# Optimization experiments

Measured on AMD Instinct MI355X. Metric: run time of the kernel, lower is better.

## Reference

```python
import jax, jax.numpy as jnp
import numpy as np

P_CLASSES = 1024   # num_classes_per_batch
K_SAMP = 4         # num_samples_per_class
MARGIN = 1.0
EPS = 1e-6
EMBED_DIM = 128


def setup_inputs() -> dict:
    key = jax.random.key(0)
    x = jax.random.normal(key, (P_CLASSES * K_SAMP, EMBED_DIM), dtype=jnp.float32)
    return {"x": x}


def reference(x):
    p, k = P_CLASSES, K_SAMP
    n = p * k
    # pairwise distances D[i,j] = sqrt(relu(|xi|^2 - 2 xi.xj + |xj|^2) + eps)
    norms = jnp.sum(x * x, axis=1)
    D = norms[:, None] - 2.0 * (x @ x.T) + norms[None, :]
    D = jnp.sqrt(jax.nn.relu(D) + EPS)  # [n, n]

    # all positive pairs (i<j) within each class, vectorized over classes
    ii, jj = np.triu_indices(k, 1)                      # [m], m = k*(k-1)/2
    c = np.arange(p)
    ri = (c[:, None] * k + ii[None, :]).reshape(-1)     # [P] = [p*m]
    rj = (c[:, None] * k + jj[None, :]).reshape(-1)
    pair_cls = np.repeat(c, len(ii))                    # class of each pair
    col_cls = np.arange(n) // k                         # class of each column
    neg_mask = jnp.asarray(pair_cls[:, None] != col_cls[None, :])  # [P, n]

    # masked logsumexp over negatives from both anchor rows (concat of the
    # two sliced rows in the original code)
    rows = jnp.concatenate([D[ri], D[rj]], axis=1)                 # [P, 2n]
    mask2 = jnp.concatenate([neg_mask, neg_mask], axis=1)
    vals = jnp.where(mask2, MARGIN - rows, -jnp.inf)
    lse = jax.scipy.special.logsumexp(vals, axis=1)                # [P]

    J = lse + D[ri, rj]
    return jnp.mean(jnp.square(jax.nn.relu(J))) / 2.0
```

## Files before the change

### kernel.cpp

```cpp
#include <hip/hip_runtime.h>

#define NROWS 4096
#define DIM 128
#define PCLS 1024
#define NPAIR 6144
#define MARGIN 1.0f
#define EPS 1e-6f

typedef __attribute__((ext_vector_type(8))) short bf16x8;
typedef __attribute__((ext_vector_type(4))) float f32x4;

union FragU { uint4 u; bf16x8 v; };

__device__ __forceinline__ unsigned short f2bf(float f) {
    unsigned int b = __float_as_uint(f);
    b = (b + 0x7FFFu + ((b >> 16) & 1u)) >> 16;
    return (unsigned short)b;
}

__global__ void prep_kernel(const float* __restrict__ x,
                            unsigned short* __restrict__ xbf,
                            float* __restrict__ norms) {
    int row = blockIdx.x * 4 + (threadIdx.x >> 6);
    int l = threadIdx.x & 63;
    float2 v = *reinterpret_cast<const float2*>(x + row * DIM + 2 * l);
    unsigned int packed = (unsigned int)f2bf(v.x) | ((unsigned int)f2bf(v.y) << 16);
    *reinterpret_cast<unsigned int*>(xbf + row * DIM + 2 * l) = packed;
    float s = v.x * v.x + v.y * v.y;
    #pragma unroll
    for (int m = 1; m < 64; m <<= 1) s += __shfl_xor(s, m, 64);
    if (l == 0) norms[row] = s;
}

__launch_bounds__(512, 4)
__global__ void main_kernel(const unsigned short* __restrict__ xbf,
                            const float* __restrict__ norms,
                            float* __restrict__ partial,
                            float* __restrict__ posD) {
    __shared__ __align__(16) unsigned short lds[256 * DIM];
    const int t = threadIdx.x;
    const int w = t >> 6;
    const int l = t & 63;
    const int rb = blockIdx.x >> 4;
    const int cs = blockIdx.x & 15;
    const int rbase = rb * 128 + w * 16;
    const int cbase = cs * 256;
    const int lg = l >> 4;
    const int lr = l & 15;

    FragU afr[4];
    const char* abase = (const char*)xbf + (size_t)(rbase + lr) * 256 + lg * 16;
    #pragma unroll
    for (int s = 0; s < 4; ++s)
        afr[s].u = *reinterpret_cast<const uint4*>(abase + s * 64);

    float njv[16];
    #pragma unroll
    for (int tile = 0; tile < 16; ++tile)
        njv[tile] = norms[cbase + tile * 16 + lr];

    float ni[4];
    #pragma unroll
    for (int rr = 0; rr < 4; ++rr) ni[rr] = norms[rbase + lg * 4 + rr];

    #pragma unroll
    for (int it = 0; it < 8; ++it) {
        int lin = it * 8192 + t * 16;
        int col = lin >> 8;
        int inner = lin & 255;
        uint4 v = *reinterpret_cast<const uint4*>(
            (const char*)xbf + (size_t)(cbase + col) * 256 + inner);
        *reinterpret_cast<uint4*>(
            (char*)lds + col * 256 + (inner ^ ((col & 7) << 4))) = v;
    }

    __syncthreads();

    float accS[4] = {0.f, 0.f, 0.f, 0.f};

    #pragma unroll
    for (int tile = 0; tile < 16; ++tile) {
        const int lcol = tile * 16 + lr;
        const float nj = njv[tile];
        const char* bbase = (const char*)lds + lcol * 256;
        const int xr = (lcol & 7) << 4;
        f32x4 acc = {0.f, 0.f, 0.f, 0.f};
        #pragma unroll
        for (int s = 0; s < 4; ++s) {
            FragU bu;
            int inner = s * 64 + lg * 16;
            bu.u = *reinterpret_cast<const uint4*>(bbase + (inner ^ xr));
            acc = __builtin_amdgcn_mfma_f32_16x16x32_bf16(afr[s].v, bu.v, acc, 0, 0, 0);
        }
        const bool diag = (cbase + tile * 16) == rbase;
        if (!diag) {
            #pragma unroll
            for (int rr = 0; rr < 4; ++rr) {
                float nn = ni[rr] + nj;
                float d2 = fmaf(-2.0f, acc[rr], nn);
                float d = __builtin_amdgcn_sqrtf(fmaxf(d2, 0.f) + EPS);
                accS[rr] += __expf(MARGIN - d);
            }
        } else {
            #pragma unroll
            for (int rr = 0; rr < 4; ++rr) {
                int a = lg * 4 + rr;
                int b = lr;
                float nn = ni[rr] + nj;
                float d2 = fmaf(-2.0f, acc[rr], nn);
                float d = __builtin_amdgcn_sqrtf(fmaxf(d2, 0.f) + EPS);
                bool same = (a >> 2) == (b >> 2);
                accS[rr] += same ? 0.f : __expf(MARGIN - d);
                if (same && a < b) {
                    int i = a & 3, j = b & 3;
                    int idx = i * (7 - i) / 2 + (j - i - 1);
                    int cls = (rbase + a) >> 2;
                    posD[cls * 6 + idx] = d;
                }
            }
        }
    }
    #pragma unroll
    for (int rr = 0; rr < 4; ++rr) {
        #pragma unroll
        for (int m = 1; m < 16; m <<= 1) accS[rr] += __shfl_xor(accS[rr], m, 64);
    }
    if (lr == 0) {
        #pragma unroll
        for (int rr = 0; rr < 4; ++rr)
            partial[cs * NROWS + rbase + lg * 4 + rr] = accS[rr];
    }
}

__global__ void tail_kernel(const float* __restrict__ partial,
                            const float* __restrict__ posD,
                            float* __restrict__ out) {
    const int c = threadIdx.x;
    float S[4] = {0.f, 0.f, 0.f, 0.f};
    #pragma unroll
    for (int sp = 0; sp < 16; ++sp) {
        float4 v = *reinterpret_cast<const float4*>(partial + sp * NROWS + 4 * c);
        S[0] += v.x; S[1] += v.y; S[2] += v.z; S[3] += v.w;
    }
    const int II[6] = {0, 0, 0, 1, 1, 2};
    const int JJ[6] = {1, 2, 3, 2, 3, 3};
    float acc = 0.f;
    #pragma unroll
    for (int p = 0; p < 6; ++p) {
        float d = posD[c * 6 + p];
        float J = __logf(S[II[p]] + S[JJ[p]]) + d;
        float r = fmaxf(J, 0.f);
        acc += r * r;
    }
    #pragma unroll
    for (int m = 1; m < 64; m <<= 1) acc += __shfl_xor(acc, m, 64);
    __shared__ float red[16];
    if ((c & 63) == 0) red[c >> 6] = acc;
    __syncthreads();
    if (c < 64) {
        float v = (c < 16) ? red[c] : 0.f;
        #pragma unroll
        for (int m = 1; m < 16; m <<= 1) v += __shfl_xor(v, m, 64);
        if (c == 0) out[0] = v * (1.0f / (2.0f * (float)NPAIR));
    }
}

extern "C" void kernel_launch(void* const* d_in, const int* in_sizes, int n_in,
                              void* d_out, int out_size, void* d_ws, size_t ws_size,
                              hipStream_t stream) {
    const float* x = (const float*)d_in[0];
    char* ws = (char*)d_ws;
    unsigned short* xbf = (unsigned short*)ws;
    float* norms = (float*)(ws + 1048576);
    float* partial = (float*)(ws + 1048576 + 16384);
    float* posD = (float*)(ws + 1048576 + 16384 + 262144);
    float* out = (float*)d_out;

    hipLaunchKernelGGL(prep_kernel, dim3(NROWS / 4), dim3(256), 0, stream, x, xbf, norms);
    hipLaunchKernelGGL(main_kernel, dim3(512), dim3(512), 0, stream, xbf, norms, partial, posD);
    hipLaunchKernelGGL(tail_kernel, dim3(1), dim3(1024), 0, stream, partial, posD, out);
}
```

Baseline: 24.60 us.

## Retile main kernel to 256x128 blocks with two row subtiles per wave

Changes the block tile from 128 rows x 256 columns to 256 rows x 128 columns, so each wave holds two 16-row A fragments and reuses every LDS B fragment for two MFMAs. The LDS footprint halves and the column split doubles to 32 slices, so the tail kernel now sums 32 partials and the posD workspace offset moves. It also folds EPS into the norms and computes exp as exp2 with a single FMA. The cost is more registers per thread under the 512x4 launch bounds and twice the partial-sum traffic.

```diff
diff --git a/kernel.cpp b/kernel.cpp
--- a/kernel.cpp
+++ b/kernel.cpp
@@ -6,6 +6,7 @@
 #define NPAIR 6144
 #define MARGIN 1.0f
 #define EPS 1e-6f
+#define LOG2E 1.4426950408889634f
 
 typedef __attribute__((ext_vector_type(8))) short bf16x8;
 typedef __attribute__((ext_vector_type(4))) float f32x4;
@@ -37,34 +38,41 @@
                             const float* __restrict__ norms,
                             float* __restrict__ partial,
                             float* __restrict__ posD) {
-    __shared__ __align__(16) unsigned short lds[256 * DIM];
+    __shared__ __align__(16) unsigned short lds[128 * DIM];
     const int t = threadIdx.x;
     const int w = t >> 6;
     const int l = t & 63;
-    const int rb = blockIdx.x >> 4;
-    const int cs = blockIdx.x & 15;
-    const int rbase = rb * 128 + w * 16;
-    const int cbase = cs * 256;
+    const int rb = blockIdx.x >> 5;
+    const int cs = blockIdx.x & 31;
+    const int rbase = rb * 256 + w * 32;
+    const int cbase = cs * 128;
     const int lg = l >> 4;
     const int lr = l & 15;
 
-    FragU afr[4];
-    const char* abase = (const char*)xbf + (size_t)(rbase + lr) * 256 + lg * 16;
+    FragU afr[8];
     #pragma unroll
-    for (int s = 0; s < 4; ++s)
-        afr[s].u = *reinterpret_cast<const uint4*>(abase + s * 64);
+    for (int sub = 0; sub < 2; ++sub) {
+        const char* abase = (const char*)xbf +
+            (size_t)(rbase + sub * 16 + lr) * 256 + lg * 16;
+        #pragma unroll
+        for (int s = 0; s < 4; ++s)
+            afr[sub * 4 + s].u = *reinterpret_cast<const uint4*>(abase + s * 64);
+    }
 
-    float njv[16];
+    float njv[8];
     #pragma unroll
-    for (int tile = 0; tile < 16; ++tile)
+    for (int tile = 0; tile < 8; ++tile)
         njv[tile] = norms[cbase + tile * 16 + lr];
 
-    float ni[4];
+    float ni[8];
     #pragma unroll
-    for (int rr = 0; rr < 4; ++rr) ni[rr] = norms[rbase + lg * 4 + rr];
+    for (int sub = 0; sub < 2; ++sub)
+        #pragma unroll
+        for (int rr = 0; rr < 4; ++rr)
+            ni[sub * 4 + rr] = norms[rbase + sub * 16 + lg * 4 + rr] + EPS;
 
     #pragma unroll
-    for (int it = 0; it < 8; ++it) {
+    for (int it = 0; it < 4; ++it) {
         int lin = it * 8192 + t * 16;
         int col = lin >> 8;
         int inner = lin & 255;
@@ -76,59 +84,68 @@
 
     __syncthreads();
 
-    float accS[4] = {0.f, 0.f, 0.f, 0.f};
+    float accS[8] = {0.f, 0.f, 0.f, 0.f, 0.f, 0.f, 0.f, 0.f};
 
     #pragma unroll
-    for (int tile = 0; tile < 16; ++tile) {
+    for (int tile = 0; tile < 8; ++tile) {
         const int lcol = tile * 16 + lr;
         const float nj = njv[tile];
         const char* bbase = (const char*)lds + lcol * 256;
         const int xr = (lcol & 7) << 4;
-        f32x4 acc = {0.f, 0.f, 0.f, 0.f};
+        f32x4 acc0 = {0.f, 0.f, 0.f, 0.f};
+        f32x4 acc1 = {0.f, 0.f, 0.f, 0.f};
         #pragma unroll
         for (int s = 0; s < 4; ++s) {
             FragU bu;
             int inner = s * 64 + lg * 16;
             bu.u = *reinterpret_cast<const uint4*>(bbase + (inner ^ xr));
-            acc = __builtin_amdgcn_mfma_f32_16x16x32_bf16(afr[s].v, bu.v, acc, 0, 0, 0);
+            acc0 = __builtin_amdgcn_mfma_f32_16x16x32_bf16(afr[s].v, bu.v, acc0, 0, 0, 0);
+            acc1 = __builtin_amdgcn_mfma_f32_16x16x32_bf16(afr[4 + s].v, bu.v, acc1, 0, 0, 0);
         }
-        const bool diag = (cbase + tile * 16) == rbase;
-        if (!diag) {
-            #pragma unroll
-            for (int rr = 0; rr < 4; ++rr) {
-                float nn = ni[rr] + nj;
-                float d2 = fmaf(-2.0f, acc[rr], nn);
-                float d = __builtin_amdgcn_sqrtf(fmaxf(d2, 0.f) + EPS);
-                accS[rr] += __expf(MARGIN - d);
-            }
-        } else {
-            #pragma unroll
-            for (int rr = 0; rr < 4; ++rr) {
-                int a = lg * 4 + rr;
-                int b = lr;
-                float nn = ni[rr] + nj;
-                float d2 = fmaf(-2.0f, acc[rr], nn);
-                float d = __builtin_amdgcn_sqrtf(fmaxf(d2, 0.f) + EPS);
-                bool same = (a >> 2) == (b >> 2);
-                accS[rr] += same ? 0.f : __expf(MARGIN - d);
-                if (same && a < b) {
-                    int i = a & 3, j = b & 3;
-                    int idx = i * (7 - i) / 2 + (j - i - 1);
-                    int cls = (rbase + a) >> 2;
-                    posD[cls * 6 + idx] = d;
+        #pragma unroll
+        for (int sub = 0; sub < 2; ++sub) {
+            const f32x4& acc = sub ? acc1 : acc0;
+            const bool diag = (cbase + tile * 16) == (rbase + sub * 16);
+            if (!diag) {
+                #pragma unroll
+                for (int rr = 0; rr < 4; ++rr) {
+                    float nn = ni[sub * 4 + rr] + nj;
+                    float d2 = fmaf(-2.0f, acc[rr], nn);
+                    float d = __builtin_amdgcn_sqrtf(fmaxf(d2, EPS));
+                    accS[sub * 4 + rr] += __builtin_amdgcn_exp2f(fmaf(d, -LOG2E, LOG2E));
+                }
+            } else {
+                #pragma unroll
+                for (int rr = 0; rr < 4; ++rr) {
+                    int a = lg * 4 + rr;
+                    int b = lr;
+                    float nn = ni[sub * 4 + rr] + nj;
+                    float d2 = fmaf(-2.0f, acc[rr], nn);
+                    float d = __builtin_amdgcn_sqrtf(fmaxf(d2, EPS));
+                    float e = __builtin_amdgcn_exp2f(fmaf(d, -LOG2E, LOG2E));
+                    bool same = (a >> 2) == (b >> 2);
+                    accS[sub * 4 + rr] += same ? 0.f : e;
+                    if (same && a < b) {
+                        int i = a & 3, j = b & 3;
+                        int idx = i * (7 - i) / 2 + (j - i - 1);
+                        int cls = (rbase + sub * 16 + a) >> 2;
+                        posD[cls * 6 + idx] = d;
+                    }
                 }
             }
         }
     }
     #pragma unroll
-    for (int rr = 0; rr < 4; ++rr) {
+    for (int i = 0; i < 8; ++i) {
         #pragma unroll
-        for (int m = 1; m < 16; m <<= 1) accS[rr] += __shfl_xor(accS[rr], m, 64);
+        for (int m = 1; m < 16; m <<= 1) accS[i] += __shfl_xor(accS[i], m, 64);
     }
     if (lr == 0) {
         #pragma unroll
-        for (int rr = 0; rr < 4; ++rr)
-            partial[cs * NROWS + rbase + lg * 4 + rr] = accS[rr];
+        for (int sub = 0; sub < 2; ++sub)
+            #pragma unroll
+            for (int rr = 0; rr < 4; ++rr)
+                partial[cs * NROWS + rbase + sub * 16 + lg * 4 + rr] = accS[sub * 4 + rr];
     }
 }
 
@@ -138,7 +155,7 @@
     const int c = threadIdx.x;
     float S[4] = {0.f, 0.f, 0.f, 0.f};
     #pragma unroll
-    for (int sp = 0; sp < 16; ++sp) {
+    for (int sp = 0; sp < 32; ++sp) {
         float4 v = *reinterpret_cast<const float4*>(partial + sp * NROWS + 4 * c);
         S[0] += v.x; S[1] += v.y; S[2] += v.z; S[3] += v.w;
     }
@@ -173,7 +190,7 @@
     unsigned short* xbf = (unsigned short*)ws;
     float* norms = (float*)(ws + 1048576);
     float* partial = (float*)(ws + 1048576 + 16384);
-    float* posD = (float*)(ws + 1048576 + 16384 + 262144);
+    float* posD = (float*)(ws + 1048576 + 16384 + 524288);
     float* out = (float*)d_out;
 
     hipLaunchKernelGGL(prep_kernel, dim3(NROWS / 4), dim3(256), 0, stream, x, xbf, norms);
```

Measured after the change: 26.88 us. 1.09x slower.

## Exploit distance matrix symmetry by computing only upper-triangular 128x128 tiles

Applied to the files above, without the earlier changes.

The main kernel now computes only the upper-triangular 128x128 blocks of the symmetric distance matrix, 528 blocks in place of 512 blocks of 128x256. Each off-diagonal block adds exp sums both across rows and down columns, with the column sums reduced across waves through shared memory. This roughly halves the MFMA and transcendental work. The exp is rewritten as exp2 with folded constants, and the partial sums are stored as bf16 to shrink the tail kernel's reads. The cost is an extra column reduction with a __syncthreads, more partial slices for the tail to sum, and bf16 rounding error in the partial sums.

```diff
diff --git a/kernel.cpp b/kernel.cpp
--- a/kernel.cpp
+++ b/kernel.cpp
@@ -6,6 +6,8 @@
 #define NPAIR 6144
 #define MARGIN 1.0f
 #define EPS 1e-6f
+#define LOG2E 1.4426950408889634f
+#define NSPLIT 32
 
 typedef __attribute__((ext_vector_type(8))) short bf16x8;
 typedef __attribute__((ext_vector_type(4))) float f32x4;
@@ -16,6 +18,9 @@
     unsigned int b = __float_as_uint(f);
     b = (b + 0x7FFFu + ((b >> 16) & 1u)) >> 16;
     return (unsigned short)b;
+}
+__device__ __forceinline__ float bf2f(unsigned short u) {
+    return __uint_as_float((unsigned int)u << 16);
 }
 
 __global__ void prep_kernel(const float* __restrict__ x,
@@ -35,36 +40,44 @@
 __launch_bounds__(512, 4)
 __global__ void main_kernel(const unsigned short* __restrict__ xbf,
                             const float* __restrict__ norms,
-                            float* __restrict__ partial,
+                            unsigned short* __restrict__ partial,
                             float* __restrict__ posD) {
-    __shared__ __align__(16) unsigned short lds[256 * DIM];
+    __shared__ __align__(16) unsigned short lds[128 * DIM];
+    __shared__ float colW[8 * 128];
     const int t = threadIdx.x;
     const int w = t >> 6;
     const int l = t & 63;
-    const int rb = blockIdx.x >> 4;
-    const int cs = blockIdx.x & 15;
-    const int rbase = rb * 128 + w * 16;
-    const int cbase = cs * 256;
     const int lg = l >> 4;
     const int lr = l & 15;
 
+    int u = blockIdx.x;
+    int rb = (int)((65.0f - sqrtf(4225.0f - 8.0f * (float)u)) * 0.5f);
+    while (rb > 0 && rb * (65 - rb) / 2 > u) --rb;
+    while ((rb + 1) * (64 - rb) / 2 <= u) ++rb;
+    const int cb = rb + (u - rb * (65 - rb) / 2);
+    const bool offd = (cb != rb);
+
+    const int rbase = rb * 128 + w * 16;
+    const int cbase = cb * 128;
+
     FragU afr[4];
     const char* abase = (const char*)xbf + (size_t)(rbase + lr) * 256 + lg * 16;
     #pragma unroll
     for (int s = 0; s < 4; ++s)
         afr[s].u = *reinterpret_cast<const uint4*>(abase + s * 64);
 
-    float njv[16];
-    #pragma unroll
-    for (int tile = 0; tile < 16; ++tile)
+    float njv[8];
+    #pragma unroll
+    for (int tile = 0; tile < 8; ++tile)
         njv[tile] = norms[cbase + tile * 16 + lr];
 
     float ni[4];
     #pragma unroll
-    for (int rr = 0; rr < 4; ++rr) ni[rr] = norms[rbase + lg * 4 + rr];
-
-    #pragma unroll
-    for (int it = 0; it < 8; ++it) {
+    for (int rr = 0; rr < 4; ++rr)
+        ni[rr] = norms[rbase + lg * 4 + rr] + EPS;
+
+    #pragma unroll
+    for (int it = 0; it < 4; ++it) {
         int lin = it * 8192 + t * 16;
         int col = lin >> 8;
         int inner = lin & 255;
@@ -77,9 +90,10 @@
     __syncthreads();
 
     float accS[4] = {0.f, 0.f, 0.f, 0.f};
-
-    #pragma unroll
-    for (int tile = 0; tile < 16; ++tile) {
+    float colA[8];
+
+    #pragma unroll
+    for (int tile = 0; tile < 8; ++tile) {
         const int lcol = tile * 16 + lr;
         const float nj = njv[tile];
         const char* bbase = (const char*)lds + lcol * 256;
@@ -92,14 +106,25 @@
             bu.u = *reinterpret_cast<const uint4*>(bbase + (inner ^ xr));
             acc = __builtin_amdgcn_mfma_f32_16x16x32_bf16(afr[s].v, bu.v, acc, 0, 0, 0);
         }
-        const bool diag = (cbase + tile * 16) == rbase;
-        if (!diag) {
+        if (offd) {
+            float es = 0.f;
             #pragma unroll
             for (int rr = 0; rr < 4; ++rr) {
                 float nn = ni[rr] + nj;
                 float d2 = fmaf(-2.0f, acc[rr], nn);
-                float d = __builtin_amdgcn_sqrtf(fmaxf(d2, 0.f) + EPS);
-                accS[rr] += __expf(MARGIN - d);
+                float d = __builtin_amdgcn_sqrtf(fmaxf(d2, EPS));
+                float e = __builtin_amdgcn_exp2f(fmaf(d, -LOG2E, LOG2E));
+                accS[rr] += e;
+                es += e;
+            }
+            colA[tile] = es;
+        } else if (tile != w) {
+            #pragma unroll
+            for (int rr = 0; rr < 4; ++rr) {
+                float nn = ni[rr] + nj;
+                float d2 = fmaf(-2.0f, acc[rr], nn);
+                float d = __builtin_amdgcn_sqrtf(fmaxf(d2, EPS));
+                accS[rr] += __builtin_amdgcn_exp2f(fmaf(d, -LOG2E, LOG2E));
             }
         } else {
             #pragma unroll
@@ -108,9 +133,10 @@
                 int b = lr;
                 float nn = ni[rr] + nj;
                 float d2 = fmaf(-2.0f, acc[rr], nn);
-                float d = __builtin_amdgcn_sqrtf(fmaxf(d2, 0.f) + EPS);
+                float d = __builtin_amdgcn_sqrtf(fmaxf(d2, EPS));
+                float e = __builtin_amdgcn_exp2f(fmaf(d, -LOG2E, LOG2E));
                 bool same = (a >> 2) == (b >> 2);
-                accS[rr] += same ? 0.f : __expf(MARGIN - d);
+                accS[rr] += same ? 0.f : e;
                 if (same && a < b) {
                     int i = a & 3, j = b & 3;
                     int idx = i * (7 - i) / 2 + (j - i - 1);
@@ -120,6 +146,7 @@
             }
         }
     }
+
     #pragma unroll
     for (int rr = 0; rr < 4; ++rr) {
         #pragma unroll
@@ -128,19 +155,39 @@
     if (lr == 0) {
         #pragma unroll
         for (int rr = 0; rr < 4; ++rr)
-            partial[cs * NROWS + rbase + lg * 4 + rr] = accS[rr];
-    }
-}
-
-__global__ void tail_kernel(const float* __restrict__ partial,
+            partial[cb * NROWS + rbase + lg * 4 + rr] = f2bf(accS[rr]);
+    }
+
+    if (offd) {
+        #pragma unroll
+        for (int tile = 0; tile < 8; ++tile) {
+            colA[tile] += __shfl_xor(colA[tile], 16, 64);
+            colA[tile] += __shfl_xor(colA[tile], 32, 64);
+        }
+        if (l < 16) {
+            #pragma unroll
+            for (int tile = 0; tile < 8; ++tile)
+                colW[w * 128 + tile * 16 + l] = colA[tile];
+        }
+        __syncthreads();
+        if (t < 128) {
+            float s = 0.f;
+            #pragma unroll
+            for (int ww = 0; ww < 8; ++ww) s += colW[ww * 128 + t];
+            partial[rb * NROWS + cbase + t] = f2bf(s);
+        }
+    }
+}
+
+__global__ void tail_kernel(const unsigned short* __restrict__ partial,
                             const float* __restrict__ posD,
                             float* __restrict__ out) {
     const int c = threadIdx.x;
     float S[4] = {0.f, 0.f, 0.f, 0.f};
     #pragma unroll
-    for (int sp = 0; sp < 16; ++sp) {
-        float4 v = *reinterpret_cast<const float4*>(partial + sp * NROWS + 4 * c);
-        S[0] += v.x; S[1] += v.y; S[2] += v.z; S[3] += v.w;
+    for (int sp = 0; sp < NSPLIT; ++sp) {
+        ushort4 v = *reinterpret_cast<const ushort4*>(partial + sp * NROWS + 4 * c);
+        S[0] += bf2f(v.x); S[1] += bf2f(v.y); S[2] += bf2f(v.z); S[3] += bf2f(v.w);
     }
     const int II[6] = {0, 0, 0, 1, 1, 2};
     const int JJ[6] = {1, 2, 3, 2, 3, 3};
@@ -172,11 +219,11 @@
     char* ws = (char*)d_ws;
     unsigned short* xbf = (unsigned short*)ws;
     float* norms = (float*)(ws + 1048576);
-    float* partial = (float*)(ws + 1048576 + 16384);
+    unsigned short* partial = (unsigned short*)(ws + 1048576 + 16384);
     float* posD = (float*)(ws + 1048576 + 16384 + 262144);
     float* out = (float*)d_out;
 
     hipLaunchKernelGGL(prep_kernel, dim3(NROWS / 4), dim3(256), 0, stream, x, xbf, norms);
-    hipLaunchKernelGGL(main_kernel, dim3(512), dim3(512), 0, stream, xbf, norms, partial, posD);
+    hipLaunchKernelGGL(main_kernel, dim3(528), dim3(512), 0, stream, xbf, norms, partial, posD);
     hipLaunchKernelGGL(tail_kernel, dim3(1), dim3(1024), 0, stream, partial, posD, out);
 }
```

Measured after the change: 25.51 us. 1.04x slower.
